# Kernel optimization log

Measured on AMD Instinct MI355X. Metric: run time of the kernel, lower is better.

## Reference

```python
import jax, jax.numpy as jnp
import numpy as np

B, L, D, H = 1, 512, 64, 64
EPS = 1e-5


def _ln(x, w, b):
    mu = jnp.mean(x, axis=-1, keepdims=True)
    var = jnp.var(x, axis=-1, keepdims=True)
    return (x - mu) * jax.lax.rsqrt(var + EPS) * w + b


def setup_inputs() -> dict:
    key = jax.random.key(0)
    ks = jax.random.split(key, 16)
    s = 0.02
    return {
        "x": jax.random.normal(ks[0], (B, L, L, D), dtype=jnp.float32),
        "sequence_mask": jax.random.randint(ks[1], (B, L), 0, 2, dtype=jnp.int32),
        "norm_w": jnp.ones((D,), jnp.float32),
        "norm_b": jnp.zeros((D,), jnp.float32),
        "left_w": jax.random.normal(ks[2], (D, H), jnp.float32) * s,
        "left_b": jnp.zeros((H,), jnp.float32),
        "right_w": jax.random.normal(ks[3], (D, H), jnp.float32) * s,
        "right_b": jnp.zeros((H,), jnp.float32),
        "lgate_w": jax.random.normal(ks[4], (D, H), jnp.float32) * s,
        "lgate_b": jnp.ones((H,), jnp.float32),
        "rgate_w": jax.random.normal(ks[5], (D, H), jnp.float32) * s,
        "rgate_b": jnp.ones((H,), jnp.float32),
        "ogate_w": jax.random.normal(ks[6], (D, D), jnp.float32) * s,
        "ogate_b": jnp.ones((D,), jnp.float32),
        "onorm_w": jnp.ones((H,), jnp.float32),
        "onorm_b": jnp.zeros((H,), jnp.float32),
        "out_w": jax.random.normal(ks[7], (H, D), jnp.float32) * s,
        "out_b": jnp.zeros((D,), jnp.float32),
    }


def reference(x, sequence_mask, norm_w, norm_b, left_w, left_b, right_w, right_b,
              lgate_w, lgate_b, rgate_w, rgate_b, ogate_w, ogate_b,
              onorm_w, onorm_b, out_w, out_b):
    xn = _ln(x, norm_w, norm_b)                              # (B,L,L,D)
    left = xn @ left_w + left_b                              # (B,L,L,H)
    right = xn @ right_w + right_b
    m = sequence_mask.astype(xn.dtype)                       # (B,L)
    mask = (m[:, :, None] * m[:, None, :])[..., None]        # (B,L,L,1)
    left = left * mask
    right = right * mask
    left = left * jax.nn.sigmoid(xn @ lgate_w + lgate_b)
    right = right * jax.nn.sigmoid(xn @ rgate_w + rgate_b)
    out_gate = jax.nn.sigmoid(xn @ ogate_w + ogate_b)        # (B,L,L,D)
    # ingoing mix: out[i,j,d] = sum_k left[k,j,d] * right[k,i,d]
    out = jnp.einsum('bkjd,bkid->bijd', left, right)         # (B,L,L,H)
    out = _ln(out, onorm_w, onorm_b)
    out = out @ out_w + out_b                                # (B,L,L,D)
    return out * out_gate
```

## Files before the change

kernel.cpp:

```cpp
#include <hip/hip_runtime.h>


typedef __attribute__((ext_vector_type(4))) float f32x4;
typedef __attribute__((ext_vector_type(8))) __bf16 bf16x8;
typedef __attribute__((ext_vector_type(2))) _Float16 h2;

__device__ __forceinline__ unsigned short f2bf(float f) {
  unsigned u = __float_as_uint(f);
  u += 0x7FFFu + ((u >> 16) & 1u);
  return (unsigned short)(u >> 16);
}
__device__ __forceinline__ float bf2f(unsigned short h) {
  return __uint_as_float(((unsigned)h) << 16);
}
__device__ __forceinline__ unsigned pk2bf(float a, float b) {
  unsigned short ua = __builtin_bit_cast(unsigned short, (__bf16)a);
  unsigned short ub = __builtin_bit_cast(unsigned short, (__bf16)b);
  return (unsigned)ua | ((unsigned)ub << 16);
}
__device__ __forceinline__ float sigm(float x) { return 1.0f / (1.0f + __expf(-x)); }

__global__ __launch_bounds__(256) void k0_prep(
    const float* __restrict__ lw, const float* __restrict__ rw,
    const float* __restrict__ lgw, const float* __restrict__ rgw,
    const float* __restrict__ ogw, unsigned short* __restrict__ wt) {
  const int t0 = blockIdx.x * 1024 + threadIdx.x;
  #pragma unroll
  for (int e = 0; e < 4; ++e) {
    int idx = t0 + e * 256;
    int n = idx >> 6, k = idx & 63;
    const float* W = (n < 64) ? lw : (n < 128) ? rw : (n < 192) ? lgw
                     : (n < 256) ? rgw : ogw;
    float v = W[k * 64 + (n & 63)];
    int el = n * 64 + ((((k >> 3) ^ (n & 7)) << 3) | (k & 7));
    wt[el] = f2bf(v);
  }
}

__global__ __launch_bounds__(512) void k1_proj(
    const float* __restrict__ x, const int* __restrict__ smask,
    const float* __restrict__ norm_w, const float* __restrict__ norm_b,
    const float* __restrict__ left_b, const float* __restrict__ right_b,
    const float* __restrict__ lgate_b, const float* __restrict__ rgate_b,
    const float* __restrict__ ogate_b, const unsigned short* __restrict__ wt,
    unsigned short* __restrict__ left_t, unsigned short* __restrict__ right_t,
    unsigned short* __restrict__ ogate) {
  __shared__ __align__(16) char ldsWt[40960];
  __shared__ __align__(16) char ldsX[16384];
  __shared__ float sNW[64], sNB[64];
  __shared__ __align__(16) float sLB[64], sRB[64], sLGB[64], sRGB[64], sOGB[64];
  __shared__ float sMK[128];

  const int t = threadIdx.x;
  const int c = blockIdx.x & 511;
  const int r0 = (blockIdx.x >> 9) << 7;

  #pragma unroll
  for (int i = 0; i < 5; ++i) {
    int u = t + i * 512;
    *(uint4*)(ldsWt + u * 16) = *(const uint4*)((const char*)wt + u * 16);
  }
  if (t < 64) {
    sNW[t] = norm_w[t]; sNB[t] = norm_b[t];
    sLB[t] = left_b[t]; sRB[t] = right_b[t];
    sLGB[t] = lgate_b[t]; sRGB[t] = rgate_b[t]; sOGB[t] = ogate_b[t];
  }
  if (t >= 64 && t < 192) sMK[t - 64] = (float)smask[r0 + (t - 64)];
  __syncthreads();

  {
    const int m = t >> 2, q = t & 3;
    const float* xp = x + ((size_t)(r0 + m) * 512 + c) * 64 + q * 16;
    float v[16];
    #pragma unroll
    for (int i = 0; i < 4; ++i) {
      float4 f = *(const float4*)(xp + i * 4);
      v[i*4+0] = f.x; v[i*4+1] = f.y; v[i*4+2] = f.z; v[i*4+3] = f.w;
    }
    float s = 0.f, ss = 0.f;
    #pragma unroll
    for (int i = 0; i < 16; ++i) { s += v[i]; ss += v[i] * v[i]; }
    s += __shfl_xor(s, 1); s += __shfl_xor(s, 2);
    ss += __shfl_xor(ss, 1); ss += __shfl_xor(ss, 2);
    const float mu = s * 0.015625f;
    const float rs = rsqrtf(ss * 0.015625f - mu * mu + 1e-5f);
    unsigned pk[8];
    #pragma unroll
    for (int i = 0; i < 8; ++i) {
      const int d0 = q * 16 + 2 * i;
      pk[i] = pk2bf((v[2*i]   - mu) * rs * sNW[d0]     + sNB[d0],
                    (v[2*i+1] - mu) * rs * sNW[d0 + 1] + sNB[d0 + 1]);
    }
    uint4 lo; lo.x = pk[0]; lo.y = pk[1]; lo.z = pk[2]; lo.w = pk[3];
    uint4 hi; hi.x = pk[4]; hi.y = pk[5]; hi.z = pk[6]; hi.w = pk[7];
    *(uint4*)(ldsX + m * 128 + (((q * 2)     ^ (m & 7)) << 4)) = lo;
    *(uint4*)(ldsX + m * 128 + (((q * 2 + 1) ^ (m & 7)) << 4)) = hi;
  }
  __syncthreads();

  const int w = t >> 6, l = t & 63, lr = l & 15, g = l >> 4;
  f32x4 acc[20];
  #pragma unroll
  for (int nf = 0; nf < 20; ++nf) acc[nf] = (f32x4){0.f, 0.f, 0.f, 0.f};
  const int rowA = w * 16 + lr;
  #pragma unroll
  for (int s = 0; s < 2; ++s) {
    const int soff = (((s * 4 + g) ^ (lr & 7)) << 4);
    bf16x8 a = *(const bf16x8*)(ldsX + rowA * 128 + soff);
    #pragma unroll
    for (int nf = 0; nf < 16; ++nf) {
      bf16x8 bb = *(const bf16x8*)(ldsWt + (nf * 16 + lr) * 128 + soff);
      acc[nf] = __builtin_amdgcn_mfma_f32_16x16x32_bf16(a, bb, acc[nf], 0, 0, 0);
    }
    #pragma unroll
    for (int nf = 16; nf < 20; ++nf) {
      bf16x8 bb = *(const bf16x8*)(ldsWt + (nf * 16 + lr) * 128 + soff);
      acc[nf] = __builtin_amdgcn_mfma_f32_16x16x32_bf16(bb, a, acc[nf], 0, 0, 0);
    }
  }
  __syncthreads();

  char* bL = ldsWt;
  char* bR = ldsWt + 17408;
  {
    const float mc = (float)smask[c];
    float mk[4];
    #pragma unroll
    for (int rr = 0; rr < 4; ++rr) mk[rr] = mc * sMK[w * 16 + g * 4 + rr];
    const int rb2 = (w * 16 + g * 4) * 2;
    #pragma unroll
    for (int nf = 0; nf < 4; ++nf) {
      const int hh = nf * 16 + lr;
      const float lb = sLB[hh], rb = sRB[hh];
      const float lgb = sLGB[hh], rgb = sRGB[hh];
      float lo[4], ro[4];
      #pragma unroll
      for (int rr = 0; rr < 4; ++rr) {
        lo[rr] = (acc[nf][rr]     + lb) * mk[rr] * sigm(acc[8  + nf][rr] + lgb);
        ro[rr] = (acc[4 + nf][rr] + rb) * mk[rr] * sigm(acc[12 + nf][rr] + rgb);
      }
      uint2 lv; lv.x = pk2bf(lo[0], lo[1]); lv.y = pk2bf(lo[2], lo[3]);
      uint2 rv; rv.x = pk2bf(ro[0], ro[1]); rv.y = pk2bf(ro[2], ro[3]);
      *(uint2*)(bL + hh * 272 + rb2) = lv;
      *(uint2*)(bR + hh * 272 + rb2) = rv;
    }
    const int rloc = w * 16 + lr;
    #pragma unroll
    for (int nf = 0; nf < 4; ++nf) {
      const int d0 = nf * 16 + g * 4;
      const float4 ob4 = *(const float4*)&sOGB[d0];
      const float g0 = sigm(acc[16 + nf][0] + ob4.x);
      const float g1 = sigm(acc[16 + nf][1] + ob4.y);
      const float g2 = sigm(acc[16 + nf][2] + ob4.z);
      const float g3 = sigm(acc[16 + nf][3] + ob4.w);
      uint2 gv; gv.x = pk2bf(g0, g1); gv.y = pk2bf(g2, g3);
      const int slot = (d0 >> 3) ^ (rloc & 7);
      *(uint2*)(ldsX + rloc * 128 + slot * 16 + (d0 & 4) * 2) = gv;
    }
  }
  __syncthreads();

  const int cx = c & 7;
  #pragma unroll
  for (int it = 0; it < 2; ++it) {
    const int idx = it * 512 + t;
    const int hh = idx >> 4, rel = idx & 15;
    const size_t goff = (size_t)hh * 524288 + (size_t)c * 1024 +
                        (size_t)(((r0 >> 3) + (rel & 8) + ((rel & 7) ^ cx)) << 4);
    *(uint4*)((char*)left_t  + goff) = *(const uint4*)(bL + hh * 272 + rel * 16);
    *(uint4*)((char*)right_t + goff) = *(const uint4*)(bR + hh * 272 + rel * 16);
  }
  #pragma unroll
  for (int it = 0; it < 2; ++it) {
    const int idx = it * 512 + t;
    const int rl = idx >> 3, ch = idx & 7;
    *(uint4*)((char*)ogate + ((size_t)(r0 + rl) * 512 + c) * 128 + ch * 16) =
        *(const uint4*)(ldsX + rl * 128 + ((ch ^ (rl & 7)) << 4));
  }
}

__global__ __launch_bounds__(512) void k2_einsum(
    const unsigned short* __restrict__ left_t,
    const unsigned short* __restrict__ right_t,
    unsigned short* __restrict__ o) {
  __shared__ __align__(16) char lds[69632];
  char* ldsA = lds;
  char* ldsB = lds + 32768;
  const int t = threadIdx.x;
  const int bid = (int)blockIdx.x;
  const int id = ((bid & 7) << 5) | (bid >> 3);
  const int d = id >> 2;
  const int i0 = ((id >> 1) & 1) * 256;
  const int j0 = (id & 1) * 256;
  const int w = t >> 6, l = t & 63, lr = l & 15, g = l >> 4;
  const char* Rb = (const char*)right_t + (size_t)d * 524288;
  const char* Lb = (const char*)left_t  + (size_t)d * 524288;
  f32x4 acc[8][4];
  #pragma unroll
  for (int mi = 0; mi < 8; ++mi)
    #pragma unroll
    for (int nj = 0; nj < 4; ++nj) acc[mi][nj] = (f32x4){0.f, 0.f, 0.f, 0.f};
  const int wm0 = (w >> 2) * 128, wn0 = (w & 3) * 64;
  for (int kb = 0; kb < 512; kb += 64) {
    #pragma unroll
    for (int cc = 0; cc < 4; ++cc) {
      const int p16 = (w * 4 + cc) * 64 + l;
      const int m = p16 >> 3, sl = p16 & 7;
      __builtin_amdgcn_global_load_lds(
          (const void*)(Rb + (size_t)(i0 + m) * 1024 + kb * 2 + sl * 16),
          (void*)(ldsA + p16 * 16), 16, 0, 0);
      __builtin_amdgcn_global_load_lds(
          (const void*)(Lb + (size_t)(j0 + m) * 1024 + kb * 2 + sl * 16),
          (void*)(ldsB + p16 * 16), 16, 0, 0);
    }
    __syncthreads();
    #pragma unroll
    for (int s = 0; s < 2; ++s) {
      const int soff = (((s * 4 + g) ^ (lr & 7)) << 4);
      bf16x8 af[8], bfr[4];
      #pragma unroll
      for (int mi = 0; mi < 8; ++mi)
        af[mi] = *(const bf16x8*)(ldsA + (wm0 + mi * 16 + lr) * 128 + soff);
      #pragma unroll
      for (int nj = 0; nj < 4; ++nj)
        bfr[nj] = *(const bf16x8*)(ldsB + (wn0 + nj * 16 + lr) * 128 + soff);
      #pragma unroll
      for (int mi = 0; mi < 8; ++mi)
        #pragma unroll
        for (int nj = 0; nj < 4; ++nj)
          acc[mi][nj] = __builtin_amdgcn_mfma_f32_16x16x32_bf16(
              af[mi], bfr[nj], acc[mi][nj], 0, 0, 0);
    }
    __syncthreads();
  }
  #pragma unroll
  for (int h2i = 0; h2i < 2; ++h2i) {
    if ((w >> 2) == h2i) {
      #pragma unroll
      for (int mi = 0; mi < 8; ++mi)
        #pragma unroll
        for (int nj = 0; nj < 4; ++nj)
          #pragma unroll
          for (int rr = 0; rr < 4; ++rr) {
            const int rl = mi * 16 + g * 4 + rr;
            const int col = wn0 + nj * 16 + lr;
            *(unsigned short*)(lds + rl * 544 + col * 2) = f2bf(acc[mi][nj][rr]);
          }
    }
    __syncthreads();
    #pragma unroll
    for (int it = 0; it < 8; ++it) {
      const int q = it * 512 + t;
      const int rl = q >> 5, ch = q & 31;
      *(uint4*)((char*)o + (size_t)d * 524288 +
                (size_t)(i0 + h2i * 128 + rl) * 1024 + (size_t)j0 * 2 + ch * 16) =
          *(const uint4*)(lds + rl * 544 + ch * 16);
    }
    __syncthreads();
  }
}

__global__ __launch_bounds__(256) void k3_final(
    const unsigned short* __restrict__ o, const unsigned short* __restrict__ ogate,
    const float* __restrict__ onorm_w, const float* __restrict__ onorm_b,
    const float* __restrict__ out_w, const float* __restrict__ out_b,
    float* __restrict__ out) {
  __shared__ __align__(16) _Float16 ldsW[64 * 72];
  __shared__ float sONW[64], sONB[64], sOB[64];
  const int t = threadIdx.x;
  const int i = blockIdx.x >> 2;
  const int j0 = (blockIdx.x & 3) << 7;
  const size_t p0 = (size_t)i * 512 + j0;
  const int p = t >> 1, h = t & 1;

  float v[32];
  {
    const unsigned short* op0 = o + (size_t)(h * 32) * 262144 + p0 + p;
    #pragma unroll
    for (int dl = 0; dl < 32; ++dl)
      v[dl] = bf2f(op0[(size_t)dl * 262144]);
  }

  #pragma unroll
  for (int e = 0; e < 16; ++e) {
    const int idx = e * 256 + t;
    ldsW[(idx >> 6) * 72 + (idx & 63)] = (_Float16)out_w[idx];
  }
  if (t < 64) { sONW[t] = onorm_w[t]; sONB[t] = onorm_b[t]; sOB[t] = out_b[t]; }
  __syncthreads();

  float s = 0.f, ss = 0.f;
  #pragma unroll
  for (int dl = 0; dl < 32; ++dl) { s += v[dl]; ss += v[dl] * v[dl]; }
  s += __shfl_xor(s, 1); ss += __shfl_xor(ss, 1);
  const float mu = s * 0.015625f;
  const float rs = rsqrtf(ss * 0.015625f - mu * mu + 1e-5f);
  float xv[32];
  #pragma unroll
  for (int dl = 0; dl < 32; ++dl) {
    const int d = h * 32 + dl;
    xv[dl] = (v[dl] - mu) * rs * sONW[d] + sONB[d];
  }

  const int n0 = h * 32;
  _Float16 xA[32], xB[32];
  #pragma unroll
  for (int dl = 0; dl < 32; ++dl) {
    xA[dl] = (_Float16)xv[dl];
    xB[dl] = (_Float16)__shfl_xor(xv[dl], 1);
  }
  float acc[32];
  #pragma unroll
  for (int n = 0; n < 32; ++n) acc[n] = 0.f;
  const int kO = h * 32, kP = (1 - h) * 32;
  #pragma unroll
  for (int pb = 0; pb < 4; ++pb) {
    h2 acc2[16];
    #pragma unroll
    for (int n2 = 0; n2 < 16; ++n2) { acc2[n2][0] = (_Float16)0.f; acc2[n2][1] = (_Float16)0.f; }
    #pragma unroll
    for (int kk = 0; kk < 16; ++kk) {
      const int ko = (pb & 1) * 16 + kk;
      const _Float16 av = (pb < 2) ? xA[ko] : xB[ko];
      const int k = ((pb < 2) ? kO : kP) + ko;
      h2 a2; a2[0] = av; a2[1] = av;
      const uint4* wr = (const uint4*)(ldsW + k * 72 + n0);
      const uint4 w0 = wr[0], w1 = wr[1], w2 = wr[2], w3 = wr[3];
      const unsigned wu[16] = {w0.x, w0.y, w0.z, w0.w, w1.x, w1.y, w1.z, w1.w,
                               w2.x, w2.y, w2.z, w2.w, w3.x, w3.y, w3.z, w3.w};
      #pragma unroll
      for (int n2 = 0; n2 < 16; ++n2)
        acc2[n2] = a2 * __builtin_bit_cast(h2, wu[n2]) + acc2[n2];
    }
    #pragma unroll
    for (int n2 = 0; n2 < 16; ++n2) {
      acc[2 * n2]     += (float)acc2[n2][0];
      acc[2 * n2 + 1] += (float)acc2[n2][1];
    }
  }

  const size_t pl = p0 + p;
  const unsigned short* gp = ogate + pl * 64 + n0;
  float* op = out + pl * 64 + n0;
  #pragma unroll
  for (int c = 0; c < 4; ++c) {
    const uint4 g4 = *(const uint4*)(gp + c * 8);
    const unsigned gg[4] = {g4.x, g4.y, g4.z, g4.w};
    float r[8];
    #pragma unroll
    for (int e = 0; e < 4; ++e) {
      r[2*e]   = (acc[c*8 + 2*e]   + sOB[n0 + c*8 + 2*e])   *
                 bf2f((unsigned short)(gg[e] & 0xffffu));
      r[2*e+1] = (acc[c*8 + 2*e+1] + sOB[n0 + c*8 + 2*e+1]) *
                 bf2f((unsigned short)(gg[e] >> 16));
    }
    float4 s0; s0.x = r[0]; s0.y = r[1]; s0.z = r[2]; s0.w = r[3];
    float4 s1; s1.x = r[4]; s1.y = r[5]; s1.z = r[6]; s1.w = r[7];
    *(float4*)(op + c * 8)     = s0;
    *(float4*)(op + c * 8 + 4) = s1;
  }
}

extern "C" void kernel_launch(void* const* d_in, const int* in_sizes, int n_in,
                              void* d_out, int out_size, void* d_ws, size_t ws_size,
                              hipStream_t stream) {
  const float* x       = (const float*)d_in[0];
  const int*   sm      = (const int*)d_in[1];
  const float* norm_w  = (const float*)d_in[2];
  const float* norm_b  = (const float*)d_in[3];
  const float* left_w  = (const float*)d_in[4];
  const float* left_b  = (const float*)d_in[5];
  const float* right_w = (const float*)d_in[6];
  const float* right_b = (const float*)d_in[7];
  const float* lgate_w = (const float*)d_in[8];
  const float* lgate_b = (const float*)d_in[9];
  const float* rgate_w = (const float*)d_in[10];
  const float* rgate_b = (const float*)d_in[11];
  const float* ogate_w = (const float*)d_in[12];
  const float* ogate_b = (const float*)d_in[13];
  const float* onorm_w = (const float*)d_in[14];
  const float* onorm_b = (const float*)d_in[15];
  const float* out_w   = (const float*)d_in[16];
  const float* out_b   = (const float*)d_in[17];

  char* ws = (char*)d_ws;
  unsigned short* left_t  = (unsigned short*)(ws + 0);
  unsigned short* right_t = (unsigned short*)(ws + 33554432);
  unsigned short* ogate   = (unsigned short*)(ws + 67108864);
  unsigned short* obuf    = (unsigned short*)(ws + 100663296);
  unsigned short* wt      = (unsigned short*)(ws + 134217728);

  if (ws_size < (size_t)134217728 + 40960) return;

  k0_prep<<<dim3(20), dim3(256), 0, stream>>>(left_w, right_w, lgate_w, rgate_w,
                                              ogate_w, wt);
  k1_proj<<<dim3(2048), dim3(512), 0, stream>>>(x, sm, norm_w, norm_b, left_b,
                                                right_b, lgate_b, rgate_b,
                                                ogate_b, wt, left_t, right_t,
                                                ogate);
  k2_einsum<<<dim3(256), dim3(512), 0, stream>>>(left_t, right_t, obuf);
  k3_final<<<dim3(2048), dim3(256), 0, stream>>>(obuf, ogate, onorm_w, onorm_b,
                                                 out_w, out_b, (float*)d_out);
}
```

Measured before the change: 120.7 us.

## Read projection weights from global memory and reuse one LDS staging buffer in k1

```diff
diff --git a/kernel.cpp b/kernel.cpp
--- a/kernel.cpp
+++ b/kernel.cpp
@@ -45,8 +45,8 @@
     const float* __restrict__ ogate_b, const unsigned short* __restrict__ wt,
     unsigned short* __restrict__ left_t, unsigned short* __restrict__ right_t,
     unsigned short* __restrict__ ogate) {
-  __shared__ __align__(16) char ldsWt[40960];
   __shared__ __align__(16) char ldsX[16384];
+  __shared__ __align__(16) char ldsB2[17408];
   __shared__ float sNW[64], sNB[64];
   __shared__ __align__(16) float sLB[64], sRB[64], sLGB[64], sRGB[64], sOGB[64];
   __shared__ float sMK[128];
@@ -55,11 +55,6 @@
   const int c = blockIdx.x & 511;
   const int r0 = (blockIdx.x >> 9) << 7;
 
-  #pragma unroll
-  for (int i = 0; i < 5; ++i) {
-    int u = t + i * 512;
-    *(uint4*)(ldsWt + u * 16) = *(const uint4*)((const char*)wt + u * 16);
-  }
   if (t < 64) {
     sNW[t] = norm_w[t]; sNB[t] = norm_b[t];
     sLB[t] = left_b[t]; sRB[t] = right_b[t];
@@ -99,6 +94,7 @@
   __syncthreads();
 
   const int w = t >> 6, l = t & 63, lr = l & 15, g = l >> 4;
+  const char* wtc = (const char*)wt;
   f32x4 acc[20];
   #pragma unroll
   for (int nf = 0; nf < 20; ++nf) acc[nf] = (f32x4){0.f, 0.f, 0.f, 0.f};
@@ -109,25 +105,23 @@
     bf16x8 a = *(const bf16x8*)(ldsX + rowA * 128 + soff);
     #pragma unroll
     for (int nf = 0; nf < 16; ++nf) {
-      bf16x8 bb = *(const bf16x8*)(ldsWt + (nf * 16 + lr) * 128 + soff);
+      bf16x8 bb = *(const bf16x8*)(wtc + (nf * 16 + lr) * 128 + soff);
       acc[nf] = __builtin_amdgcn_mfma_f32_16x16x32_bf16(a, bb, acc[nf], 0, 0, 0);
     }
     #pragma unroll
     for (int nf = 16; nf < 20; ++nf) {
-      bf16x8 bb = *(const bf16x8*)(ldsWt + (nf * 16 + lr) * 128 + soff);
+      bf16x8 bb = *(const bf16x8*)(wtc + (nf * 16 + lr) * 128 + soff);
       acc[nf] = __builtin_amdgcn_mfma_f32_16x16x32_bf16(bb, a, acc[nf], 0, 0, 0);
     }
   }
   __syncthreads();
 
-  char* bL = ldsWt;
-  char* bR = ldsWt + 17408;
+  uint2 lpk[4], rpk[4];
   {
     const float mc = (float)smask[c];
     float mk[4];
     #pragma unroll
     for (int rr = 0; rr < 4; ++rr) mk[rr] = mc * sMK[w * 16 + g * 4 + rr];
-    const int rb2 = (w * 16 + g * 4) * 2;
     #pragma unroll
     for (int nf = 0; nf < 4; ++nf) {
       const int hh = nf * 16 + lr;
@@ -139,11 +133,13 @@
         lo[rr] = (acc[nf][rr]     + lb) * mk[rr] * sigm(acc[8  + nf][rr] + lgb);
         ro[rr] = (acc[4 + nf][rr] + rb) * mk[rr] * sigm(acc[12 + nf][rr] + rgb);
       }
-      uint2 lv; lv.x = pk2bf(lo[0], lo[1]); lv.y = pk2bf(lo[2], lo[3]);
-      uint2 rv; rv.x = pk2bf(ro[0], ro[1]); rv.y = pk2bf(ro[2], ro[3]);
-      *(uint2*)(bL + hh * 272 + rb2) = lv;
-      *(uint2*)(bR + hh * 272 + rb2) = rv;
-    }
+      lpk[nf].x = pk2bf(lo[0], lo[1]); lpk[nf].y = pk2bf(lo[2], lo[3]);
+      rpk[nf].x = pk2bf(ro[0], ro[1]); rpk[nf].y = pk2bf(ro[2], ro[3]);
+    }
+    const int rb2 = (w * 16 + g * 4) * 2;
+    #pragma unroll
+    for (int nf = 0; nf < 4; ++nf)
+      *(uint2*)(ldsB2 + (nf * 16 + lr) * 272 + rb2) = lpk[nf];
     const int rloc = w * 16 + lr;
     #pragma unroll
     for (int nf = 0; nf < 4; ++nf) {
@@ -167,8 +163,7 @@
     const int hh = idx >> 4, rel = idx & 15;
     const size_t goff = (size_t)hh * 524288 + (size_t)c * 1024 +
                         (size_t)(((r0 >> 3) + (rel & 8) + ((rel & 7) ^ cx)) << 4);
-    *(uint4*)((char*)left_t  + goff) = *(const uint4*)(bL + hh * 272 + rel * 16);
-    *(uint4*)((char*)right_t + goff) = *(const uint4*)(bR + hh * 272 + rel * 16);
+    *(uint4*)((char*)left_t + goff) = *(const uint4*)(ldsB2 + hh * 272 + rel * 16);
   }
   #pragma unroll
   for (int it = 0; it < 2; ++it) {
@@ -176,6 +171,23 @@
     const int rl = idx >> 3, ch = idx & 7;
     *(uint4*)((char*)ogate + ((size_t)(r0 + rl) * 512 + c) * 128 + ch * 16) =
         *(const uint4*)(ldsX + rl * 128 + ((ch ^ (rl & 7)) << 4));
+  }
+  __syncthreads();
+
+  {
+    const int rb2 = (w * 16 + g * 4) * 2;
+    #pragma unroll
+    for (int nf = 0; nf < 4; ++nf)
+      *(uint2*)(ldsB2 + (nf * 16 + lr) * 272 + rb2) = rpk[nf];
+  }
+  __syncthreads();
+  #pragma unroll
+  for (int it = 0; it < 2; ++it) {
+    const int idx = it * 512 + t;
+    const int hh = idx >> 4, rel = idx & 15;
+    const size_t goff = (size_t)hh * 524288 + (size_t)c * 1024 +
+                        (size_t)(((r0 >> 3) + (rel & 8) + ((rel & 7) ^ cx)) << 4);
+    *(uint4*)((char*)right_t + goff) = *(const uint4*)(ldsB2 + hh * 272 + rel * 16);
   }
 }
 
```

Measured after the change: 159.2 us. +31.9%, slower.
